# Kernel optimization log

Hardware: AMD Instinct MI355X
Metric: run time of the kernel (lower is better)

The kernel has to match this reference:

```python
import jax, jax.numpy as jnp
import numpy as np

N = 50000          # nodes
E = 800000         # edges
D_IN, D_HID, D_OUT = 256, 128, 64
NUM_GRAPHS = 16
BN_EPS = 1e-5


def gcn_conv(x, src, dst, W, b, n_nodes):
    """PyG GCNConv: add self-loops, sym-normalized aggregation, then bias."""
    loop = jnp.arange(n_nodes, dtype=src.dtype)
    s = jnp.concatenate([src, loop])
    d = jnp.concatenate([dst, loop])
    deg = jax.ops.segment_sum(jnp.ones_like(s, dtype=x.dtype), d, num_segments=n_nodes)
    dinv = jax.lax.rsqrt(jnp.maximum(deg, 1.0))  # deg >= 1 due to self-loops
    norm = dinv[s] * dinv[d]                      # [E+N]
    h = x @ W                                     # [N, out]
    msg = h[s] * norm[:, None]                    # gather + scale
    out = jax.ops.segment_sum(msg, d, num_segments=n_nodes)
    return out + b


def batch_norm(x, gamma, beta):
    mu = jnp.mean(x, axis=0)
    var = jnp.mean(jnp.square(x - mu), axis=0)
    return (x - mu) * jax.lax.rsqrt(var + BN_EPS) * gamma + beta


def setup_inputs() -> dict:
    key = jax.random.key(0)
    ks = jax.random.split(key, 10)
    x = jax.random.normal(ks[0], (N, D_IN), dtype=jnp.float32)
    edge_index = jax.random.randint(ks[1], (2, E), 0, N, dtype=jnp.int64)
    batch = jnp.sort(jax.random.randint(ks[2], (N,), 0, NUM_GRAPHS, dtype=jnp.int64))
    def glorot(k, fan_in, fan_out):
        lim = np.sqrt(6.0 / (fan_in + fan_out))
        return jax.random.uniform(k, (fan_in, fan_out), jnp.float32, -lim, lim)
    return {
        "x": x, "edge_index": edge_index, "batch": batch,
        "W1": glorot(ks[3], D_IN, D_HID),  "b1": jnp.zeros((D_HID,), jnp.float32),
        "W2": glorot(ks[4], D_HID, D_HID), "b2": jnp.zeros((D_HID,), jnp.float32),
        "W3": glorot(ks[5], D_HID, D_OUT), "b3": jnp.zeros((D_OUT,), jnp.float32),
        "g1": jnp.ones((D_HID,), jnp.float32), "be1": jnp.zeros((D_HID,), jnp.float32),
        "g2": jnp.ones((D_HID,), jnp.float32), "be2": jnp.zeros((D_HID,), jnp.float32),
    }


def reference(x, edge_index, batch, W1, b1, W2, b2, W3, b3, g1, be1, g2, be2):
    src, dst = edge_index[0], edge_index[1]
    n = x.shape[0]
    h = gcn_conv(x, src, dst, W1, b1, n)
    h = jax.nn.relu(batch_norm(h, g1, be1))
    h = gcn_conv(h, src, dst, W2, b2, n)
    h = jax.nn.relu(batch_norm(h, g2, be2))
    h = gcn_conv(h, src, dst, W3, b3, n)          # [N, D_OUT]
    # global mean pool over graph ids
    sums = jax.ops.segment_sum(h, batch, num_segments=NUM_GRAPHS)
    cnts = jax.ops.segment_sum(jnp.ones((n,), h.dtype), batch, num_segments=NUM_GRAPHS)
    return sums / jnp.maximum(cnts, 1.0)[:, None]  # [NUM_GRAPHS, D_OUT]
```

## Files before the change

kernel.cpp:

```cpp
#include <hip/hip_runtime.h>
#include <hip/hip_bf16.h>

#define D_IN   256
#define D_HID  128
#define D_OUT_ 64
#define NGRAPH 16
#define BN_EPS 1e-5f

#define SCAN_TPB 256
#define SCAN_VPT 4

typedef __attribute__((ext_vector_type(8))) short short8;
typedef __attribute__((ext_vector_type(4))) float floatx4;

__device__ __forceinline__ unsigned short f2bf(float x) {
    unsigned u = __float_as_uint(x);
    return (unsigned short)((u + 0x7fffu + ((u >> 16) & 1u)) >> 16);
}
__device__ __forceinline__ unsigned pack2bf(float lo, float hi) {
    return (unsigned)f2bf(lo) | ((unsigned)f2bf(hi) << 16);
}
__device__ __forceinline__ void bf2_decode(unsigned u, float& lo, float& hi) {
    lo = __uint_as_float(u << 16);
    hi = __uint_as_float(u & 0xffff0000u);
}
__device__ __forceinline__ void accum8(float* acc, uint4 qv, float wt) {
    float f0,f1,f2,f3,f4,f5,f6,f7;
    bf2_decode(qv.x, f0, f1); bf2_decode(qv.y, f2, f3);
    bf2_decode(qv.z, f4, f5); bf2_decode(qv.w, f6, f7);
    acc[0]=fmaf(f0,wt,acc[0]); acc[1]=fmaf(f1,wt,acc[1]);
    acc[2]=fmaf(f2,wt,acc[2]); acc[3]=fmaf(f3,wt,acc[3]);
    acc[4]=fmaf(f4,wt,acc[4]); acc[5]=fmaf(f5,wt,acc[5]);
    acc[6]=fmaf(f6,wt,acc[6]); acc[7]=fmaf(f7,wt,acc[7]);
}

__global__ void count_deg_kernel(const int* __restrict__ dst, int E, int* __restrict__ deg) {
    int e = blockIdx.x * blockDim.x + threadIdx.x;
    if (e < E) atomicAdd(&deg[dst[e]], 1);
}

__global__ void dinv_kernel(const int* __restrict__ deg, int N, float* __restrict__ dinv) {
    int v = blockIdx.x * blockDim.x + threadIdx.x;
    if (v < N) dinv[v] = rsqrtf((float)(deg[v] + 1));
}

__global__ void block_sum_kernel(const int* __restrict__ deg, int N, int* __restrict__ bsum) {
    __shared__ int red[SCAN_TPB];
    int t = threadIdx.x;
    int base = blockIdx.x * (SCAN_TPB * SCAN_VPT) + t;
    int s = 0;
    #pragma unroll
    for (int i = 0; i < SCAN_VPT; ++i) {
        int idx = base + i * SCAN_TPB;
        if (idx < N) s += deg[idx];
    }
    red[t] = s;
    __syncthreads();
    for (int off = SCAN_TPB / 2; off > 0; off >>= 1) {
        if (t < off) red[t] += red[t + off];
        __syncthreads();
    }
    if (t == 0) bsum[blockIdx.x] = red[0];
}

__global__ void scan_bsum_kernel(const int* __restrict__ bsum, int NB,
                                 int* __restrict__ bprefix,
                                 int* __restrict__ rowstart, int N, int E) {
    __shared__ int part[SCAN_TPB];
    int t = threadIdx.x;
    int s = (t < NB) ? bsum[t] : 0;
    part[t] = s;
    __syncthreads();
    for (int off = 1; off < SCAN_TPB; off <<= 1) {
        int x = (t >= off) ? part[t - off] : 0;
        __syncthreads();
        part[t] += x;
        __syncthreads();
    }
    if (t < NB) bprefix[t] = part[t] - s;
    if (t == 0) rowstart[N] = E;
}

__global__ void local_scan_kernel(const int* __restrict__ deg, int N,
                                  const int* __restrict__ bprefix,
                                  int* __restrict__ rowstart) {
    __shared__ int part[SCAN_TPB];
    int t = threadIdx.x;
    int base = blockIdx.x * (SCAN_TPB * SCAN_VPT) + t * SCAN_VPT;
    int v[SCAN_VPT];
    int s = 0;
    #pragma unroll
    for (int i = 0; i < SCAN_VPT; ++i) {
        v[i] = (base + i < N) ? deg[base + i] : 0;
        s += v[i];
    }
    part[t] = s;
    __syncthreads();
    for (int off = 1; off < SCAN_TPB; off <<= 1) {
        int x = (t >= off) ? part[t - off] : 0;
        __syncthreads();
        part[t] += x;
        __syncthreads();
    }
    int excl = part[t] - s + bprefix[blockIdx.x];
    #pragma unroll
    for (int i = 0; i < SCAN_VPT; ++i) {
        if (base + i < N) rowstart[base + i] = excl;
        excl += v[i];
    }
}

__global__ void wprep_kernel(const float* __restrict__ W, int K, int NOUT,
                             unsigned short* __restrict__ Wt) {
    int idx = blockIdx.x * blockDim.x + threadIdx.x;
    if (idx >= K * NOUT) return;
    int k = idx / NOUT, n = idx - k * NOUT;
    Wt[(size_t)n * K + k] = f2bf(W[idx]);
}

template<int K, int NOUT, int FUSE, int ABF16>
__device__ __forceinline__ void gemm_body(
        int bid, const void* __restrict__ Aptr, const unsigned short* __restrict__ Wt,
        unsigned short* __restrict__ Cb, int M,
        const float* __restrict__ sums, const float* __restrict__ sumsq,
        const float* __restrict__ gam, const float* __restrict__ bet, float invN) {
    constexpr int NT = NOUT / 16;
    constexpr int KS = K / 32;
    __shared__ float s_sc[FUSE ? K : 1];
    __shared__ float s_sh[FUSE ? K : 1];
    if (FUSE) {
        int t = threadIdx.x;
        if (t < K) {
            float mu  = sums[t] * invN;
            float var = sumsq[t] * invN - mu * mu;
            float sc  = gam[t] * rsqrtf(var + BN_EPS);
            s_sc[t] = sc;
            s_sh[t] = fmaf(-mu, sc, bet[t]);
        }
        __syncthreads();
    }
    int lane = threadIdx.x & 63;
    int wave = threadIdx.x >> 6;
    int col  = lane & 15;
    int quad = lane >> 4;
    int kq   = quad * 8;
    int row  = bid * 64 + wave * 16 + col;
    int rowc = min(row, M - 1);

    short8 afr[KS];
    if (ABF16) {
        const unsigned short* Ab = (const unsigned short*)Aptr;
        uint4 q[KS];
        #pragma unroll
        for (int i = 0; i < KS; ++i)
            q[i] = *(const uint4*)&Ab[(size_t)rowc * K + i * 32 + kq];
        #pragma unroll
        for (int i = 0; i < KS; ++i) {
            if (FUSE) {
                int kb = i * 32 + kq;
                float f0,f1,f2,f3,f4,f5,f6,f7;
                bf2_decode(q[i].x, f0, f1); bf2_decode(q[i].y, f2, f3);
                bf2_decode(q[i].z, f4, f5); bf2_decode(q[i].w, f6, f7);
                float4 sc0 = *(const float4*)&s_sc[kb];
                float4 sc1 = *(const float4*)&s_sc[kb + 4];
                float4 sh0 = *(const float4*)&s_sh[kb];
                float4 sh1 = *(const float4*)&s_sh[kb + 4];
                f0 = fmaxf(0.f, fmaf(f0, sc0.x, sh0.x));
                f1 = fmaxf(0.f, fmaf(f1, sc0.y, sh0.y));
                f2 = fmaxf(0.f, fmaf(f2, sc0.z, sh0.z));
                f3 = fmaxf(0.f, fmaf(f3, sc0.w, sh0.w));
                f4 = fmaxf(0.f, fmaf(f4, sc1.x, sh1.x));
                f5 = fmaxf(0.f, fmaf(f5, sc1.y, sh1.y));
                f6 = fmaxf(0.f, fmaf(f6, sc1.z, sh1.z));
                f7 = fmaxf(0.f, fmaf(f7, sc1.w, sh1.w));
                uint4 p;
                p.x = pack2bf(f0, f1); p.y = pack2bf(f2, f3);
                p.z = pack2bf(f4, f5); p.w = pack2bf(f6, f7);
                afr[i] = __builtin_bit_cast(short8, p);
            } else {
                afr[i] = __builtin_bit_cast(short8, q[i]);
            }
        }
    } else {
        const float* Af = (const float*)Aptr;
        float4 a0[KS], a1[KS];
        #pragma unroll
        for (int i = 0; i < KS; ++i) {
            a0[i] = *(const float4*)&Af[(size_t)rowc * K + i * 32 + kq];
            a1[i] = *(const float4*)&Af[(size_t)rowc * K + i * 32 + kq + 4];
        }
        #pragma unroll
        for (int i = 0; i < KS; ++i) {
            uint4 p;
            p.x = pack2bf(a0[i].x, a0[i].y); p.y = pack2bf(a0[i].z, a0[i].w);
            p.z = pack2bf(a1[i].x, a1[i].y); p.w = pack2bf(a1[i].z, a1[i].w);
            afr[i] = __builtin_bit_cast(short8, p);
        }
    }

    floatx4 acc[NT];
    #pragma unroll
    for (int nt = 0; nt < NT; ++nt) acc[nt] = (floatx4){0.f, 0.f, 0.f, 0.f};

    #pragma unroll
    for (int i = 0; i < KS; ++i) {
        #pragma unroll
        for (int nt = 0; nt < NT; ++nt) {
            short8 bfrag = *(const short8*)&Wt[(size_t)(nt * 16 + col) * K + i * 32 + kq];
            acc[nt] = __builtin_amdgcn_mfma_f32_16x16x32_bf16(afr[i], bfrag, acc[nt], 0, 0, 0);
        }
    }

    int obase = bid * 64 + wave * 16 + quad * 4;
    #pragma unroll
    for (int r = 0; r < 4; ++r) {
        int orow = obase + r;
        if (orow < M) {
            #pragma unroll
            for (int nt = 0; nt < NT; ++nt)
                Cb[(size_t)orow * NOUT + nt * 16 + col] = f2bf(acc[nt][r]);
        }
    }
}

template<int K, int NOUT, int FUSE, int ABF16>
__global__ __launch_bounds__(256, 3) void gemm_mfma_kernel(
        const void* __restrict__ Aptr, const unsigned short* __restrict__ Wt,
        unsigned short* __restrict__ Cb, int M,
        const float* __restrict__ sums, const float* __restrict__ sumsq,
        const float* __restrict__ gam, const float* __restrict__ bet, float invN) {
    gemm_body<K, NOUT, FUSE, ABF16>(blockIdx.x, Aptr, Wt, Cb, M, sums, sumsq, gam, bet, invN);
}

__global__ __launch_bounds__(256, 3) void gemm1_scatter_kernel(
        const float* __restrict__ x, const unsigned short* __restrict__ Wt1,
        unsigned short* __restrict__ Cb, int M, int GB,
        const int* __restrict__ src, const int* __restrict__ dst, int E,
        const int* __restrict__ rowstart, int* __restrict__ cursor,
        int* __restrict__ csr) {
    if ((int)blockIdx.x < GB) {
        gemm_body<D_IN, D_HID, 0, 0>(blockIdx.x, x, Wt1, Cb, M,
                                     nullptr, nullptr, nullptr, nullptr, 0.f);
    } else {
        int e = ((int)blockIdx.x - GB) * 256 + threadIdx.x;
        if (e < E) {
            int s = src[e], d = dst[e];
            int pos = rowstart[d] + atomicAdd(&cursor[d], 1);
            csr[pos] = s;
        }
    }
}

template<int D>
__global__ __launch_bounds__(256) void agg_bf16_kernel(
        const unsigned short* __restrict__ h, const float* __restrict__ dinv,
        const int* __restrict__ rowstart, const int* __restrict__ csr,
        const float* __restrict__ bias,
        unsigned short* __restrict__ outb, int N) {
    constexpr int LPR = D / 8;
    constexpr int RPB = 256 / LPR;
    int lane = threadIdx.x & (LPR - 1);
    int r    = threadIdx.x / LPR;
    int v = blockIdx.x * RPB + r;
    if (v >= N) return;
    int c0 = lane * 8;
    const unsigned short* hc = h + c0;
    float dv = dinv[v];

    float acc[8];
    {
        float w = dv * dv;
        uint4 q = *(const uint4*)&hc[(size_t)v * D];
        float4 b0 = *(const float4*)&bias[c0];
        float4 b1 = *(const float4*)&bias[c0 + 4];
        acc[0]=b0.x; acc[1]=b0.y; acc[2]=b0.z; acc[3]=b0.w;
        acc[4]=b1.x; acc[5]=b1.y; acc[6]=b1.z; acc[7]=b1.w;
        accum8(acc, q, w);
    }

    int j  = rowstart[v];
    int j1 = rowstart[v + 1];
    for (; j + 4 <= j1; j += 4) {
        int s0 = csr[j],     s1 = csr[j + 1];
        int s2 = csr[j + 2], s3 = csr[j + 3];
        float w0 = dinv[s0] * dv, w1 = dinv[s1] * dv;
        float w2 = dinv[s2] * dv, w3 = dinv[s3] * dv;
        uint4 q0 = *(const uint4*)&hc[(size_t)s0 * D];
        uint4 q1 = *(const uint4*)&hc[(size_t)s1 * D];
        uint4 q2 = *(const uint4*)&hc[(size_t)s2 * D];
        uint4 q3 = *(const uint4*)&hc[(size_t)s3 * D];
        accum8(acc, q0, w0); accum8(acc, q1, w1);
        accum8(acc, q2, w2); accum8(acc, q3, w3);
    }
    for (; j < j1; ++j) {
        int s = csr[j];
        float w = dinv[s] * dv;
        uint4 q = *(const uint4*)&hc[(size_t)s * D];
        accum8(acc, q, w);
    }

    uint4 o;
    o.x = pack2bf(acc[0], acc[1]); o.y = pack2bf(acc[2], acc[3]);
    o.z = pack2bf(acc[4], acc[5]); o.w = pack2bf(acc[6], acc[7]);
    *(uint4*)&outb[(size_t)v * D + c0] = o;
}

__global__ void bn_stats_bf16_kernel(const unsigned short* __restrict__ x, int N,
                                     float* __restrict__ sums, float* __restrict__ sumsq) {
    __shared__ float ls0[256], ls1[256], lq0[256], lq1[256];
    int pr = threadIdx.x & 63;
    int rg = threadIdx.x >> 6;
    float s0=0.f, s1=0.f, q0=0.f, q1=0.f;
    for (int v = blockIdx.x * 4 + rg; v < N; v += gridDim.x * 4) {
        unsigned u = *(const unsigned*)&x[(size_t)v * 128 + pr * 2];
        float lo, hi; bf2_decode(u, lo, hi);
        s0 += lo; s1 += hi;
        q0 = fmaf(lo, lo, q0); q1 = fmaf(hi, hi, q1);
    }
    ls0[threadIdx.x]=s0; ls1[threadIdx.x]=s1; lq0[threadIdx.x]=q0; lq1[threadIdx.x]=q1;
    __syncthreads();
    if (threadIdx.x < 64) {
        int pp = threadIdx.x;
        float a0=0,a1=0,b0=0,b1=0;
        #pragma unroll
        for (int g = 0; g < 4; ++g) {
            a0 += ls0[g*64+pp]; a1 += ls1[g*64+pp];
            b0 += lq0[g*64+pp]; b1 += lq1[g*64+pp];
        }
        atomicAdd(&sums[pp*2],  a0); atomicAdd(&sums[pp*2+1],  a1);
        atomicAdd(&sumsq[pp*2], b0); atomicAdd(&sumsq[pp*2+1], b1);
    }
}

__global__ void pool_bf16_kernel(const unsigned short* __restrict__ x,
                                 const int* __restrict__ batch, int N,
                                 float* __restrict__ psum, int* __restrict__ pcnt) {
    __shared__ float ls[NGRAPH * 64];
    __shared__ int   lc[NGRAPH];
    for (int i = threadIdx.x; i < NGRAPH * 64; i += blockDim.x) ls[i] = 0.f;
    if (threadIdx.x < NGRAPH) lc[threadIdx.x] = 0;
    __syncthreads();
    int total = N * 32;
    for (int idx = blockIdx.x * blockDim.x + threadIdx.x; idx < total;
         idx += gridDim.x * blockDim.x) {
        int v = idx >> 5, cp = idx & 31;
        unsigned u = *(const unsigned*)&x[(size_t)v * 64 + cp * 2];
        float lo, hi; bf2_decode(u, lo, hi);
        int g = batch[v];
        atomicAdd(&ls[g * 64 + cp * 2],     lo);
        atomicAdd(&ls[g * 64 + cp * 2 + 1], hi);
        if (cp == 0) atomicAdd(&lc[g], 1);
    }
    __syncthreads();
    for (int i = threadIdx.x; i < NGRAPH * 64; i += blockDim.x) atomicAdd(&psum[i], ls[i]);
    if (threadIdx.x < NGRAPH) atomicAdd(&pcnt[threadIdx.x], lc[threadIdx.x]);
}

__global__ void pool_final_kernel(const float* __restrict__ psum, const int* __restrict__ pcnt,
                                  float* __restrict__ out) {
    int i = threadIdx.x;
    int g = i >> 6;
    float cnt = (float)max(pcnt[g], 1);
    out[i] = psum[i] / cnt;
}

extern "C" void kernel_launch(void* const* d_in, const int* in_sizes, int n_in,
                              void* d_out, int out_size, void* d_ws, size_t ws_size,
                              hipStream_t stream) {
    const float* x   = (const float*)d_in[0];
    const int*   ei  = (const int*)d_in[1];
    const int*   bat = (const int*)d_in[2];
    const float* W1  = (const float*)d_in[3];
    const float* b1  = (const float*)d_in[4];
    const float* W2  = (const float*)d_in[5];
    const float* b2  = (const float*)d_in[6];
    const float* W3  = (const float*)d_in[7];
    const float* b3  = (const float*)d_in[8];
    const float* g1  = (const float*)d_in[9];
    const float* be1 = (const float*)d_in[10];
    const float* g2  = (const float*)d_in[11];
    const float* be2 = (const float*)d_in[12];
    float* out = (float*)d_out;

    int N = in_sizes[0] / D_IN;
    int E = in_sizes[1] / 2;
    const int* src = ei;
    const int* dst = ei + E;

    char* p = (char*)d_ws;
    auto alloc = [&](size_t bytes) { char* r = p; p += (bytes + 255) & ~(size_t)255; return r; };
    int NB = (N + SCAN_TPB * SCAN_VPT - 1) / (SCAN_TPB * SCAN_VPT);
    int*   deg      = (int*)  alloc((size_t)N * 4);
    int*   rowstart = (int*)  alloc((size_t)(N + 1) * 4);
    int*   cursor   = (int*)  alloc((size_t)N * 4);
    float* dinv     = (float*)alloc((size_t)N * 4);
    int*   bsum     = (int*)  alloc((size_t)NB * 4);
    int*   bprefix  = (int*)  alloc((size_t)NB * 4);
    int*   csr      = (int*)  alloc((size_t)E * 4);
    unsigned short* hb16   = (unsigned short*)alloc((size_t)N * 128 * 2);
    unsigned short* aggb16 = (unsigned short*)alloc((size_t)N * 128 * 2);
    unsigned short* Wt1 = (unsigned short*)alloc((size_t)D_HID * D_IN * 2);
    unsigned short* Wt2 = (unsigned short*)alloc((size_t)D_HID * D_HID * 2);
    unsigned short* Wt3 = (unsigned short*)alloc((size_t)D_OUT_ * D_HID * 2);
    float* sums     = (float*)alloc(128 * 4);
    float* sumsq    = (float*)alloc(128 * 4);
    float* psum     = (float*)alloc(NGRAPH * 64 * 4);
    int*   pcnt     = (int*)  alloc(NGRAPH * 4);

    int tpb = 256;
    int ebl = (E + tpb - 1) / tpb;
    int nbl = (N + tpb - 1) / tpb;
    int gblocks = (N + 63) / 64;
    float invN = 1.0f / (float)N;

    wprep_kernel<<<(D_IN * D_HID + 255) / 256, 256, 0, stream>>>(W1, D_IN, D_HID, Wt1);
    wprep_kernel<<<(D_HID * D_HID + 255) / 256, 256, 0, stream>>>(W2, D_HID, D_HID, Wt2);
    wprep_kernel<<<(D_HID * D_OUT_ + 255) / 256, 256, 0, stream>>>(W3, D_HID, D_OUT_, Wt3);

    (void)hipMemsetAsync(deg, 0, (size_t)N * 4, stream);
    (void)hipMemsetAsync(cursor, 0, (size_t)N * 4, stream);
    count_deg_kernel<<<ebl, tpb, 0, stream>>>(dst, E, deg);
    dinv_kernel<<<nbl, tpb, 0, stream>>>(deg, N, dinv);
    block_sum_kernel<<<NB, SCAN_TPB, 0, stream>>>(deg, N, bsum);
    scan_bsum_kernel<<<1, SCAN_TPB, 0, stream>>>(bsum, NB, bprefix, rowstart, N, E);
    local_scan_kernel<<<NB, SCAN_TPB, 0, stream>>>(deg, N, bprefix, rowstart);

    gemm1_scatter_kernel<<<gblocks + ebl, 256, 0, stream>>>(
        x, Wt1, hb16, N, gblocks, src, dst, E, rowstart, cursor, csr);

    agg_bf16_kernel<D_HID><<<(N + 15) / 16, 256, 0, stream>>>(
        hb16, dinv, rowstart, csr, b1, aggb16, N);
    (void)hipMemsetAsync(sums, 0, 128 * 4, stream);
    (void)hipMemsetAsync(sumsq, 0, 128 * 4, stream);
    bn_stats_bf16_kernel<<<256, 256, 0, stream>>>(aggb16, N, sums, sumsq);

    gemm_mfma_kernel<D_HID, D_HID, 1, 1><<<gblocks, 256, 0, stream>>>(
        aggb16, Wt2, hb16, N, sums, sumsq, g1, be1, invN);
    agg_bf16_kernel<D_HID><<<(N + 15) / 16, 256, 0, stream>>>(
        hb16, dinv, rowstart, csr, b2, aggb16, N);
    (void)hipMemsetAsync(sums, 0, 128 * 4, stream);
    (void)hipMemsetAsync(sumsq, 0, 128 * 4, stream);
    bn_stats_bf16_kernel<<<256, 256, 0, stream>>>(aggb16, N, sums, sumsq);

    gemm_mfma_kernel<D_HID, D_OUT_, 1, 1><<<gblocks, 256, 0, stream>>>(
        aggb16, Wt3, hb16, N, sums, sumsq, g2, be2, invN);
    agg_bf16_kernel<D_OUT_><<<(N + 31) / 32, 256, 0, stream>>>(
        hb16, dinv, rowstart, csr, b3, aggb16, N);

    (void)hipMemsetAsync(psum, 0, NGRAPH * 64 * 4, stream);
    (void)hipMemsetAsync(pcnt, 0, NGRAPH * 4, stream);
    pool_bf16_kernel<<<256, 256, 0, stream>>>(aggb16, bat, N, psum, pcnt);
    pool_final_kernel<<<1, NGRAPH * 64, 0, stream>>>(psum, pcnt, out);
}
```

Measured before the change: 413.4 us.

## Fuse BN statistics into aggregation and precompute edge ranks during degree count

Batch-norm column sums and sums of squares are now accumulated inside the aggregation kernel through a shared-memory reduction and atomics, which removes the separate bn_stats pass that re-read the bf16 activations. The degree-count kernel now records each edge's atomic rank, so the CSR scatter writes directly without a second atomic cursor, at the cost of an extra E-sized int array. Scheduling barriers are also added after the GEMM A-loads to keep the loads grouped ahead of the conversion code. The fused stats use per-block atomics on 128 columns, and the result now depends on rank consistency.

```diff
diff --git a/kernel.cpp b/kernel.cpp
--- a/kernel.cpp
+++ b/kernel.cpp
@@ -34,9 +34,10 @@
     acc[6]=fmaf(f6,wt,acc[6]); acc[7]=fmaf(f7,wt,acc[7]);
 }
 
-__global__ void count_deg_kernel(const int* __restrict__ dst, int E, int* __restrict__ deg) {
+__global__ void count_rank_kernel(const int* __restrict__ dst, int E,
+                                  int* __restrict__ deg, int* __restrict__ rank) {
     int e = blockIdx.x * blockDim.x + threadIdx.x;
-    if (e < E) atomicAdd(&deg[dst[e]], 1);
+    if (e < E) rank[e] = atomicAdd(&deg[dst[e]], 1);
 }
 
 __global__ void dinv_kernel(const int* __restrict__ deg, int N, float* __restrict__ dinv) {
@@ -154,6 +155,7 @@
         #pragma unroll
         for (int i = 0; i < KS; ++i)
             q[i] = *(const uint4*)&Ab[(size_t)rowc * K + i * 32 + kq];
+        __builtin_amdgcn_sched_barrier(0);
         #pragma unroll
         for (int i = 0; i < KS; ++i) {
             if (FUSE) {
@@ -189,6 +191,7 @@
             a0[i] = *(const float4*)&Af[(size_t)rowc * K + i * 32 + kq];
             a1[i] = *(const float4*)&Af[(size_t)rowc * K + i * 32 + kq + 4];
         }
+        __builtin_amdgcn_sched_barrier(0);
         #pragma unroll
         for (int i = 0; i < KS; ++i) {
             uint4 p;
@@ -236,7 +239,7 @@
         const float* __restrict__ x, const unsigned short* __restrict__ Wt1,
         unsigned short* __restrict__ Cb, int M, int GB,
         const int* __restrict__ src, const int* __restrict__ dst, int E,
-        const int* __restrict__ rowstart, int* __restrict__ cursor,
+        const int* __restrict__ rowstart, const int* __restrict__ rank,
         int* __restrict__ csr) {
     if ((int)blockIdx.x < GB) {
         gemm_body<D_IN, D_HID, 0, 0>(blockIdx.x, x, Wt1, Cb, M,
@@ -244,91 +247,85 @@
     } else {
         int e = ((int)blockIdx.x - GB) * 256 + threadIdx.x;
         if (e < E) {
-            int s = src[e], d = dst[e];
-            int pos = rowstart[d] + atomicAdd(&cursor[d], 1);
-            csr[pos] = s;
-        }
-    }
-}
-
-template<int D>
+            int d = dst[e];
+            csr[rowstart[d] + rank[e]] = src[e];
+        }
+    }
+}
+
+template<int D, int BNF>
 __global__ __launch_bounds__(256) void agg_bf16_kernel(
         const unsigned short* __restrict__ h, const float* __restrict__ dinv,
         const int* __restrict__ rowstart, const int* __restrict__ csr,
         const float* __restrict__ bias,
-        unsigned short* __restrict__ outb, int N) {
+        unsigned short* __restrict__ outb, int N,
+        float* __restrict__ sums, float* __restrict__ sumsq) {
     constexpr int LPR = D / 8;
     constexpr int RPB = 256 / LPR;
     int lane = threadIdx.x & (LPR - 1);
     int r    = threadIdx.x / LPR;
     int v = blockIdx.x * RPB + r;
-    if (v >= N) return;
     int c0 = lane * 8;
-    const unsigned short* hc = h + c0;
-    float dv = dinv[v];
-
-    float acc[8];
-    {
-        float w = dv * dv;
-        uint4 q = *(const uint4*)&hc[(size_t)v * D];
-        float4 b0 = *(const float4*)&bias[c0];
-        float4 b1 = *(const float4*)&bias[c0 + 4];
-        acc[0]=b0.x; acc[1]=b0.y; acc[2]=b0.z; acc[3]=b0.w;
-        acc[4]=b1.x; acc[5]=b1.y; acc[6]=b1.z; acc[7]=b1.w;
-        accum8(acc, q, w);
-    }
-
-    int j  = rowstart[v];
-    int j1 = rowstart[v + 1];
-    for (; j + 4 <= j1; j += 4) {
-        int s0 = csr[j],     s1 = csr[j + 1];
-        int s2 = csr[j + 2], s3 = csr[j + 3];
-        float w0 = dinv[s0] * dv, w1 = dinv[s1] * dv;
-        float w2 = dinv[s2] * dv, w3 = dinv[s3] * dv;
-        uint4 q0 = *(const uint4*)&hc[(size_t)s0 * D];
-        uint4 q1 = *(const uint4*)&hc[(size_t)s1 * D];
-        uint4 q2 = *(const uint4*)&hc[(size_t)s2 * D];
-        uint4 q3 = *(const uint4*)&hc[(size_t)s3 * D];
-        accum8(acc, q0, w0); accum8(acc, q1, w1);
-        accum8(acc, q2, w2); accum8(acc, q3, w3);
-    }
-    for (; j < j1; ++j) {
-        int s = csr[j];
-        float w = dinv[s] * dv;
-        uint4 q = *(const uint4*)&hc[(size_t)s * D];
-        accum8(acc, q, w);
-    }
-
-    uint4 o;
-    o.x = pack2bf(acc[0], acc[1]); o.y = pack2bf(acc[2], acc[3]);
-    o.z = pack2bf(acc[4], acc[5]); o.w = pack2bf(acc[6], acc[7]);
-    *(uint4*)&outb[(size_t)v * D + c0] = o;
-}
-
-__global__ void bn_stats_bf16_kernel(const unsigned short* __restrict__ x, int N,
-                                     float* __restrict__ sums, float* __restrict__ sumsq) {
-    __shared__ float ls0[256], ls1[256], lq0[256], lq1[256];
-    int pr = threadIdx.x & 63;
-    int rg = threadIdx.x >> 6;
-    float s0=0.f, s1=0.f, q0=0.f, q1=0.f;
-    for (int v = blockIdx.x * 4 + rg; v < N; v += gridDim.x * 4) {
-        unsigned u = *(const unsigned*)&x[(size_t)v * 128 + pr * 2];
-        float lo, hi; bf2_decode(u, lo, hi);
-        s0 += lo; s1 += hi;
-        q0 = fmaf(lo, lo, q0); q1 = fmaf(hi, hi, q1);
-    }
-    ls0[threadIdx.x]=s0; ls1[threadIdx.x]=s1; lq0[threadIdx.x]=q0; lq1[threadIdx.x]=q1;
-    __syncthreads();
-    if (threadIdx.x < 64) {
-        int pp = threadIdx.x;
-        float a0=0,a1=0,b0=0,b1=0;
-        #pragma unroll
-        for (int g = 0; g < 4; ++g) {
-            a0 += ls0[g*64+pp]; a1 += ls1[g*64+pp];
-            b0 += lq0[g*64+pp]; b1 += lq1[g*64+pp];
-        }
-        atomicAdd(&sums[pp*2],  a0); atomicAdd(&sums[pp*2+1],  a1);
-        atomicAdd(&sumsq[pp*2], b0); atomicAdd(&sumsq[pp*2+1], b1);
+
+    float acc[8] = {0.f,0.f,0.f,0.f,0.f,0.f,0.f,0.f};
+    if (v < N) {
+        const unsigned short* hc = h + c0;
+        float dv = dinv[v];
+        {
+            float w = dv * dv;
+            uint4 q = *(const uint4*)&hc[(size_t)v * D];
+            float4 b0 = *(const float4*)&bias[c0];
+            float4 b1 = *(const float4*)&bias[c0 + 4];
+            acc[0]=b0.x; acc[1]=b0.y; acc[2]=b0.z; acc[3]=b0.w;
+            acc[4]=b1.x; acc[5]=b1.y; acc[6]=b1.z; acc[7]=b1.w;
+            accum8(acc, q, w);
+        }
+        int j  = rowstart[v];
+        int j1 = rowstart[v + 1];
+        for (; j + 4 <= j1; j += 4) {
+            int s0 = csr[j],     s1 = csr[j + 1];
+            int s2 = csr[j + 2], s3 = csr[j + 3];
+            float w0 = dinv[s0] * dv, w1 = dinv[s1] * dv;
+            float w2 = dinv[s2] * dv, w3 = dinv[s3] * dv;
+            uint4 q0 = *(const uint4*)&hc[(size_t)s0 * D];
+            uint4 q1 = *(const uint4*)&hc[(size_t)s1 * D];
+            uint4 q2 = *(const uint4*)&hc[(size_t)s2 * D];
+            uint4 q3 = *(const uint4*)&hc[(size_t)s3 * D];
+            accum8(acc, q0, w0); accum8(acc, q1, w1);
+            accum8(acc, q2, w2); accum8(acc, q3, w3);
+        }
+        for (; j < j1; ++j) {
+            int s = csr[j];
+            float w = dinv[s] * dv;
+            uint4 q = *(const uint4*)&hc[(size_t)s * D];
+            accum8(acc, q, w);
+        }
+        uint4 o;
+        o.x = pack2bf(acc[0], acc[1]); o.y = pack2bf(acc[2], acc[3]);
+        o.z = pack2bf(acc[4], acc[5]); o.w = pack2bf(acc[6], acc[7]);
+        *(uint4*)&outb[(size_t)v * D + c0] = o;
+    }
+
+    if (BNF) {
+        __shared__ float lsum[16 * 132];
+        __shared__ float lsq [16 * 132];
+        #pragma unroll
+        for (int i = 0; i < 8; ++i) {
+            lsum[r * 132 + c0 + i] = acc[i];
+            lsq [r * 132 + c0 + i] = acc[i] * acc[i];
+        }
+        __syncthreads();
+        int c = threadIdx.x;
+        if (c < 128) {
+            float s = 0.f, q = 0.f;
+            #pragma unroll
+            for (int rr = 0; rr < 16; ++rr) {
+                s += lsum[rr * 132 + c];
+                q += lsq [rr * 132 + c];
+            }
+            atomicAdd(&sums[c],  s);
+            atomicAdd(&sumsq[c], q);
+        }
     }
 }
 
@@ -392,7 +389,7 @@
     int NB = (N + SCAN_TPB * SCAN_VPT - 1) / (SCAN_TPB * SCAN_VPT);
     int*   deg      = (int*)  alloc((size_t)N * 4);
     int*   rowstart = (int*)  alloc((size_t)(N + 1) * 4);
-    int*   cursor   = (int*)  alloc((size_t)N * 4);
+    int*   rank     = (int*)  alloc((size_t)E * 4);
     float* dinv     = (float*)alloc((size_t)N * 4);
     int*   bsum     = (int*)  alloc((size_t)NB * 4);
     int*   bprefix  = (int*)  alloc((size_t)NB * 4);
@@ -418,34 +415,31 @@
     wprep_kernel<<<(D_HID * D_OUT_ + 255) / 256, 256, 0, stream>>>(W3, D_HID, D_OUT_, Wt3);
 
     (void)hipMemsetAsync(deg, 0, (size_t)N * 4, stream);
-    (void)hipMemsetAsync(cursor, 0, (size_t)N * 4, stream);
-    count_deg_kernel<<<ebl, tpb, 0, stream>>>(dst, E, deg);
+    (void)hipMemsetAsync(sums, 0, 128 * 4, stream);
+    (void)hipMemsetAsync(sumsq, 0, 128 * 4, stream);
+    count_rank_kernel<<<ebl, tpb, 0, stream>>>(dst, E, deg, rank);
     dinv_kernel<<<nbl, tpb, 0, stream>>>(deg, N, dinv);
     block_sum_kernel<<<NB, SCAN_TPB, 0, stream>>>(deg, N, bsum);
     scan_bsum_kernel<<<1, SCAN_TPB, 0, stream>>>(bsum, NB, bprefix, rowstart, N, E);
     local_scan_kernel<<<NB, SCAN_TPB, 0, stream>>>(deg, N, bprefix, rowstart);
 
     gemm1_scatter_kernel<<<gblocks + ebl, 256, 0, stream>>>(
-        x, Wt1, hb16, N, gblocks, src, dst, E, rowstart, cursor, csr);
-
-    agg_bf16_kernel<D_HID><<<(N + 15) / 16, 256, 0, stream>>>(
-        hb16, dinv, rowstart, csr, b1, aggb16, N);
+        x, Wt1, hb16, N, gblocks, src, dst, E, rowstart, rank, csr);
+
+    agg_bf16_kernel<D_HID, 1><<<(N + 15) / 16, 256, 0, stream>>>(
+        hb16, dinv, rowstart, csr, b1, aggb16, N, sums, sumsq);
+
+    gemm_mfma_kernel<D_HID, D_HID, 1, 1><<<gblocks, 256, 0, stream>>>(
+        aggb16, Wt2, hb16, N, sums, sumsq, g1, be1, invN);
     (void)hipMemsetAsync(sums, 0, 128 * 4, stream);
     (void)hipMemsetAsync(sumsq, 0, 128 * 4, stream);
-    bn_stats_bf16_kernel<<<256, 256, 0, stream>>>(aggb16, N, sums, sumsq);
-
-    gemm_mfma_kernel<D_HID, D_HID, 1, 1><<<gblocks, 256, 0, stream>>>(
-        aggb16, Wt2, hb16, N, sums, sumsq, g1, be1, invN);
-    agg_bf16_kernel<D_HID><<<(N + 15) / 16, 256, 0, stream>>>(
-        hb16, dinv, rowstart, csr, b2, aggb16, N);
-    (void)hipMemsetAsync(sums, 0, 128 * 4, stream);
-    (void)hipMemsetAsync(sumsq, 0, 128 * 4, stream);
-    bn_stats_bf16_kernel<<<256, 256, 0, stream>>>(aggb16, N, sums, sumsq);
+    agg_bf16_kernel<D_HID, 1><<<(N + 15) / 16, 256, 0, stream>>>(
+        hb16, dinv, rowstart, csr, b2, aggb16, N, sums, sumsq);
 
     gemm_mfma_kernel<D_HID, D_OUT_, 1, 1><<<gblocks, 256, 0, stream>>>(
         aggb16, Wt3, hb16, N, sums, sumsq, g2, be2, invN);
-    agg_bf16_kernel<D_OUT_><<<(N + 31) / 32, 256, 0, stream>>>(
-        hb16, dinv, rowstart, csr, b3, aggb16, N);
+    agg_bf16_kernel<D_OUT_, 0><<<(N + 31) / 32, 256, 0, stream>>>(
+        hb16, dinv, rowstart, csr, b3, aggb16, N, nullptr, nullptr);
 
     (void)hipMemsetAsync(psum, 0, NGRAPH * 64 * 4, stream);
     (void)hipMemsetAsync(pcnt, 0, NGRAPH * 4, stream);
```

New measurement: 467.8 us. +13.2%, slower.
